# Performance work log

Hardware: AMD Instinct MI355X
Metric: run time of the kernel (lower is better)

Reference implementation:

```python
import jax, jax.numpy as jnp
import numpy as np

TEMP = 0.025
BN_EPS = 1e-5


def _attention(a, W_in, b_in, g, beta, rm, rv, W_out, b_out):
    # a: (b, n1, n2, P, Q); 1x1 conv over the Q 'channel' dim, gate, softmax over P.
    m = a.mean(axis=3)                                   # (b,n1,n2,Q)
    t = jnp.einsum('bnmq,kq->bnmk', m, W_in) + b_in      # (b,n1,n2,K)
    t = jax.nn.relu((t - rm) / jnp.sqrt(rv + BN_EPS) * g + beta)
    t = jnp.einsum('bnmk,qk->bnmq', t, W_out) + b_out    # (b,n1,n2,Q)
    s = jnp.mean(a * t[:, :, :, None, :], axis=-1)       # (b,n1,n2,P)
    return jax.nn.softmax(s / TEMP, axis=-1) + 1.0


def _cam_forward(zf, xf, conv1_w, conv1_b, bn1_g, bn1_b, bn1_rm, bn1_rv,
                 conv2_w, conv2_b, conv3_w, conv3_b, bn3_g, bn3_b, bn3_rm, bn3_rv,
                 conv4_w, conv4_b):
    out1, out2 = [], []
    L = zf.shape[0]
    for l in range(L):  # small fixed loop over feature levels
        f1, f2 = zf[l], xf[l]
        b, c, h1, w1 = f1.shape
        h2, w2 = f2.shape[2], f2.shape[3]
        P, Q = h1 * w1, h2 * w2
        f1s = jnp.stack([f1.reshape(b, c, P)] * 2, axis=1)   # (b,2,c,P)
        f2s = jnp.stack([f2.reshape(b, c, Q)] * 2, axis=1)   # (b,2,c,Q)
        f1n = f1s / jnp.maximum(jnp.linalg.norm(f1s, axis=2, keepdims=True), 1e-12)
        f2n = f2s / jnp.maximum(jnp.linalg.norm(f2s, axis=2, keepdims=True), 1e-12)
        a1 = jnp.einsum('bncp,bmcq->bnmpq', f1n, f2n)        # (b,2,2,P,Q)
        att1 = _attention(a1, conv1_w, conv1_b, bn1_g, bn1_b, bn1_rm, bn1_rv,
                          conv2_w, conv2_b)                  # (b,2,2,P)
        att2 = _attention(a1.swapaxes(3, 4), conv3_w, conv3_b, bn3_g, bn3_b,
                          bn3_rm, bn3_rv, conv4_w, conv4_b)  # (b,2,2,Q)
        # mean over the (n1,n2)=(2,2) pair grid without materializing (b,2,2,c,HW)
        o1 = jnp.einsum('bncp,bnmp->bcp', f1s, att1) / 4.0
        o2 = jnp.einsum('bmcq,bnmq->bcq', f2s, att2) / 4.0
        out1.append(o1.reshape(b, c, h1, w1))
        out2.append(o2.reshape(b, c, h2, w2))
    return (jnp.stack(out1), jnp.stack(out2))


def setup_inputs() -> dict:
    key = jax.random.key(0)
    ks = jax.random.split(key, 12)
    L, B, C = 3, 32, 256
    inp = {
        'zf': jax.random.normal(ks[0], (L, B, C, 7, 7), jnp.float32),
        'xf': jax.random.normal(ks[1], (L, B, C, 31, 31), jnp.float32),
        'conv1_w': jax.random.normal(ks[2], (31, 961), jnp.float32) * np.sqrt(2.0 / 31),
        'conv1_b': jax.random.normal(ks[3], (31,), jnp.float32) * 0.05,
        'bn1_g': jax.random.uniform(ks[4], (31,), jnp.float32, 0.5, 1.5),
        'bn1_b': jax.random.normal(ks[5], (31,), jnp.float32) * 0.05,
        'bn1_rm': jnp.zeros((31,), jnp.float32),
        'bn1_rv': jnp.ones((31,), jnp.float32),
        'conv2_w': jax.random.normal(ks[6], (961, 31), jnp.float32) * np.sqrt(2.0 / 961),
        'conv2_b': jax.random.normal(ks[7], (961,), jnp.float32) * 0.05,
        'conv3_w': jax.random.normal(ks[8], (7, 49), jnp.float32) * np.sqrt(2.0 / 7),
        'conv3_b': jax.random.normal(ks[9], (7,), jnp.float32) * 0.05,
        'bn3_g': jax.random.uniform(ks[10], (7,), jnp.float32, 0.5, 1.5),
        'bn3_b': jax.random.normal(ks[11], (7,), jnp.float32) * 0.05,
        'bn3_rm': jnp.zeros((7,), jnp.float32),
        'bn3_rv': jnp.ones((7,), jnp.float32),
        'conv4_w': jax.random.normal(jax.random.fold_in(key, 100), (49, 7), jnp.float32) * np.sqrt(2.0 / 49),
        'conv4_b': jax.random.normal(jax.random.fold_in(key, 101), (49,), jnp.float32) * 0.05,
    }
    return inp


def reference(zf, xf, conv1_w, conv1_b, bn1_g, bn1_b, bn1_rm, bn1_rv,
              conv2_w, conv2_b, conv3_w, conv3_b, bn3_g, bn3_b, bn3_rm, bn3_rv,
              conv4_w, conv4_b):
    return _cam_forward(zf, xf, conv1_w, conv1_b, bn1_g, bn1_b, bn1_rm, bn1_rv,
                        conv2_w, conv2_b, conv3_w, conv3_b, bn3_g, bn3_b,
                        bn3_rm, bn3_rv, conv4_w, conv4_b)
```

## Files before the change

kernel.cpp:

```cpp
#include <hip/hip_runtime.h>
#include <math.h>

#define NLB 96
#define CC  256
#define PP  49
#define QQ  961
#define QP  1024
#define TEMP_INV 40.0f
#define BN_EPS 1e-5f

#define N1 (NLB*CC*PP)
#define N2 (NLB*CC*QQ)

__global__ __launch_bounds__(256) void prep_z(
    const float* __restrict__ zf, float* __restrict__ inv1_ws,
    float* __restrict__ w_ws)
{
    const int lb = blockIdx.x;
    const int tid = threadIdx.x;
    __shared__ float f1L[CC * PP];
    __shared__ float inv1L[PP];
    const float* __restrict__ f1 = zf + (size_t)lb * CC * PP;
    for (int i = tid; i < CC * PP; i += 256) f1L[i] = f1[i];
    __syncthreads();
    if (tid < PP) {
        float ss = 0.f;
        for (int c = 0; c < CC; ++c) { const float x = f1L[c * PP + tid]; ss = fmaf(x, x, ss); }
        const float iv = 1.0f / fmaxf(sqrtf(ss), 1e-12f);
        inv1L[tid] = iv;
        inv1_ws[lb * 64 + tid] = iv;
    }
    __syncthreads();
    {
        float s = 0.f;
#pragma unroll
        for (int p = 0; p < PP; ++p) s = fmaf(inv1L[p], f1L[tid * PP + p], s);
        w_ws[lb * CC + tid] = s;
    }
}

__global__ __launch_bounds__(256) void xpass1(
    const float* __restrict__ xf, const float* __restrict__ w_ws,
    float* __restrict__ ssp, float* __restrict__ dcp)
{
    const int qg = blockIdx.x;
    const int ch = blockIdx.y;
    const int lb = blockIdx.z;
    const int tid = threadIdx.x;
    const int q  = qg * 256 + tid;
    const bool qv = (q < QQ);
    const int qc = qv ? q : QQ - 1;

    __shared__ float wL[128];
    if (tid < 128) wL[tid] = w_ws[lb * CC + ch * 128 + tid];
    __syncthreads();

    const float* __restrict__ base =
        xf + (size_t)lb * CC * QQ + (size_t)(ch * 128) * QQ + qc;

    float ss = 0.f, dc = 0.f;
    for (int c0 = 0; c0 < 128; c0 += 16) {
        float x[16];
#pragma unroll
        for (int j = 0; j < 16; ++j) x[j] = base[(size_t)(c0 + j) * QQ];
#pragma unroll
        for (int j = 0; j < 16; ++j) {
            ss = fmaf(x[j], x[j], ss);
            dc = fmaf(wL[c0 + j], x[j], dc);
        }
    }
    if (qv) {
        ssp[((size_t)ch * NLB + lb) * QP + q] = ss;
        dcp[((size_t)ch * NLB + lb) * QP + q] = dc;
    }
}

__global__ __launch_bounds__(1024) void finq_kernel(
    const float* __restrict__ ssp, const float* __restrict__ dcp,
    float* __restrict__ inv2_ws, float* __restrict__ mcol_ws)
{
    const int lb = blockIdx.x;
    const int q = threadIdx.x;
    if (q >= QQ) return;
    const float ss = ssp[((size_t)0 * NLB + lb) * QP + q] +
                     ssp[((size_t)1 * NLB + lb) * QP + q];
    const float dc = dcp[((size_t)0 * NLB + lb) * QP + q] +
                     dcp[((size_t)1 * NLB + lb) * QP + q];
    const float iv2 = 1.0f / fmaxf(sqrtf(ss), 1e-12f);
    inv2_ws[lb * QP + q] = iv2;
    mcol_ws[lb * QP + q] = dc * iv2 * (1.0f / PP);
}

__global__ __launch_bounds__(512) void vpass_kernel(
    const float* __restrict__ xf, const float* __restrict__ wq_ws,
    float* __restrict__ vout_ws)
{
    const int cb = blockIdx.x;
    const int lb = blockIdx.y;
    const int tid  = threadIdx.x;
    const int lane = tid & 63;
    const int wave = tid >> 6;

    __shared__ float wqL[QP];
    for (int i = tid; i < QP; i += 512)
        wqL[i] = (i < QQ) ? wq_ws[lb * QP + i] : 0.f;
    __syncthreads();

    const float* __restrict__ f2 = xf + (size_t)lb * CC * QQ;

#pragma unroll
    for (int r = 0; r < 8; ++r) {
        const int c = cb * 64 + wave * 8 + r;
        const float* __restrict__ row = f2 + (size_t)c * QQ;
        float x[16];
#pragma unroll
        for (int j = 0; j < 16; ++j) {
            const int qi = j * 64 + lane;
            x[j] = row[qi < QQ ? qi : QQ - 1];
        }
        float s = 0.f;
#pragma unroll
        for (int j = 0; j < 16; ++j) s = fmaf(x[j], wqL[j * 64 + lane], s);
        for (int off = 32; off > 0; off >>= 1) s += __shfl_xor(s, off, 64);
        if (lane == 0) vout_ws[lb * CC + c] = s;
    }
}

__global__ __launch_bounds__(512) void mid_kernel(
    const float* __restrict__ zf, const float* __restrict__ v_ws,
    const float* __restrict__ inv1_ws, const float* __restrict__ mcol_ws,
    const float* __restrict__ inv2_ws,
    const float* __restrict__ W1, const float* __restrict__ b1,
    const float* __restrict__ g1, const float* __restrict__ bb1,
    const float* __restrict__ rm1, const float* __restrict__ rv1,
    const float* __restrict__ W2, const float* __restrict__ b2,
    const float* __restrict__ W3, const float* __restrict__ b3,
    const float* __restrict__ g3, const float* __restrict__ bb3,
    const float* __restrict__ rm3, const float* __restrict__ rv3,
    const float* __restrict__ W4, const float* __restrict__ b4,
    float* __restrict__ wgt_ws, float* __restrict__ wb_ws)
{
    const int lb = blockIdx.x;
    const int tid = threadIdx.x;
    __shared__ float f1L[CC * PP];
    __shared__ float inv1L[64], vL[CC], mrowL[PP];
    __shared__ float mcolL[QQ];
    __shared__ float taL[31], tbL[7], t2bL[PP];

    const float* __restrict__ f1 = zf + (size_t)lb * CC * PP;
    for (int i = tid; i < CC * PP; i += 512) f1L[i] = f1[i];
    if (tid < 64) inv1L[tid] = inv1_ws[lb * 64 + tid];
    if (tid >= 64 && tid < 64 + CC) vL[tid - 64] = v_ws[lb * CC + tid - 64];
    for (int q = tid; q < QQ; q += 512) mcolL[q] = mcol_ws[lb * QP + q];
    __syncthreads();

    if (tid < PP) {
        float s = 0.f;
        for (int c = 0; c < CC; ++c) s = fmaf(f1L[c * PP + tid], vL[c], s);
        mrowL[tid] = s * inv1L[tid] * (1.0f / QQ);
    }
    if (tid < 31 * 16) {
        const int k = tid >> 4, sub = tid & 15;
        float s = 0.f;
        for (int q = sub; q < QQ; q += 16) s = fmaf(mcolL[q], W1[k * QQ + q], s);
        s += __shfl_xor(s, 1, 64); s += __shfl_xor(s, 2, 64);
        s += __shfl_xor(s, 4, 64); s += __shfl_xor(s, 8, 64);
        if (sub == 0) {
            float t = s + b1[k];
            t = (t - rm1[k]) * rsqrtf(rv1[k] + BN_EPS) * g1[k] + bb1[k];
            taL[k] = fmaxf(t, 0.f);
        }
    }
    __syncthreads();
    if (tid < 7 * 8) {
        const int k = tid >> 3, sub = tid & 7;
        float s = 0.f;
        for (int p = sub; p < PP; p += 8) s = fmaf(mrowL[p], W3[k * PP + p], s);
        s += __shfl_xor(s, 1, 64); s += __shfl_xor(s, 2, 64); s += __shfl_xor(s, 4, 64);
        if (sub == 0) {
            float t = s + b3[k];
            t = (t - rm3[k]) * rsqrtf(rv3[k] + BN_EPS) * g3[k] + bb3[k];
            tbL[k] = fmaxf(t, 0.f);
        }
    }
    __syncthreads();
    if (tid < PP) {
        float s = b4[tid];
#pragma unroll
        for (int k = 0; k < 7; ++k) s = fmaf(tbL[k], W4[tid * 7 + k], s);
        t2bL[tid] = s;
    }
    for (int q = tid; q < QQ; q += 512) {
        float s = b2[q];
#pragma unroll
        for (int k = 0; k < 31; ++k) s = fmaf(taL[k], W2[q * 31 + k], s);
        wgt_ws[lb * QP + q] = s * inv2_ws[lb * QP + q];
    }
    __syncthreads();
    if (tid < CC) {
        float s = 0.f;
#pragma unroll
        for (int p = 0; p < PP; ++p) s = fmaf(inv1L[p] * t2bL[p], f1L[tid * PP + p], s);
        wb_ws[lb * CC + tid] = s;
    }
}

__global__ __launch_bounds__(256) void xjoint(
    const float* __restrict__ xf, const float* __restrict__ wb_ws,
    const float* __restrict__ wgt_ws,
    float* __restrict__ s2p, float* __restrict__ vbp)
{
    const int qg = blockIdx.x;
    const int ch = blockIdx.y;
    const int lb = blockIdx.z;
    const int tid  = threadIdx.x;
    const int lane = tid & 63;
    const int wave = tid >> 6;
    const int q  = qg * 256 + tid;
    const bool qv = (q < QQ);
    const int qc = qv ? q : QQ - 1;

    __shared__ float wbL[128];
    __shared__ float wgtL[256];
    __shared__ __align__(16) float tile[16 * 264];

    if (tid < 128) wbL[tid] = wb_ws[lb * CC + ch * 128 + tid];
    wgtL[tid] = qv ? wgt_ws[lb * QP + q] : 0.f;

    const float* __restrict__ base =
        xf + (size_t)lb * CC * QQ + (size_t)(ch * 128) * QQ + qc;
    float* __restrict__ vbpo = vbp + ((size_t)(lb * 4 + qg)) * CC + ch * 128;

    float dwb = 0.f;
    for (int c0 = 0; c0 < 128; c0 += 16) {
        __syncthreads();
#pragma unroll
        for (int r = 0; r < 16; ++r)
            tile[r * 264 + tid] = base[(size_t)(c0 + r) * QQ];
        __syncthreads();
#pragma unroll
        for (int r = 0; r < 16; ++r)
            dwb = fmaf(wbL[c0 + r], tile[r * 264 + tid], dwb);
#pragma unroll
        for (int rr = 0; rr < 4; ++rr) {
            const int r = wave + rr * 4;
            float s = 0.f;
#pragma unroll
            for (int j = 0; j < 4; ++j)
                s = fmaf(tile[r * 264 + j * 64 + lane], wgtL[j * 64 + lane], s);
            for (int off = 32; off > 0; off >>= 1) s += __shfl_xor(s, off, 64);
            if (lane == 0) vbpo[c0 + r] = s;
        }
    }
    if (qv) s2p[((size_t)ch * NLB + lb) * QP + q] = dwb;
}

__global__ __launch_bounds__(512) void fin_kernel(
    const float* __restrict__ zf, const float* __restrict__ vbp,
    const float* __restrict__ inv1_ws, const float* __restrict__ s2p,
    const float* __restrict__ inv2_ws,
    float* __restrict__ att1_ws, float* __restrict__ att2_ws)
{
    const int lb = blockIdx.x;
    const int tid = threadIdx.x;
    const int lane = tid & 63;
    const int wv = tid >> 6;
    __shared__ float f1L[CC * PP];
    __shared__ float vbL[CC], inv1L[64], s1L[PP];
    __shared__ float s2L[QQ];
    __shared__ float redM[8], redS[8];

    const float* __restrict__ f1 = zf + (size_t)lb * CC * PP;
    for (int i = tid; i < CC * PP; i += 512) f1L[i] = f1[i];
    if (tid < CC) {
        float s = 0.f;
#pragma unroll
        for (int qg = 0; qg < 4; ++qg)
            s += vbp[((size_t)(lb * 4 + qg)) * CC + tid];
        vbL[tid] = s;
    }
    if (tid >= 256 && tid < 320) inv1L[tid - 256] = inv1_ws[lb * 64 + tid - 256];
    for (int q = tid; q < QQ; q += 512)
        s2L[q] = (s2p[((size_t)0 * NLB + lb) * QP + q] +
                  s2p[((size_t)1 * NLB + lb) * QP + q]) *
                 inv2_ws[lb * QP + q] * (1.0f / PP) * TEMP_INV;
    __syncthreads();

    if (tid < PP) {
        float s = 0.f;
        for (int c = 0; c < CC; ++c) s = fmaf(f1L[c * PP + tid], vbL[c], s);
        s1L[tid] = s * inv1L[tid] * (1.0f / QQ) * TEMP_INV;
    }
    __syncthreads();

    if (wv == 0) {
        const float v = (lane < PP) ? s1L[lane] : -3.4e38f;
        float m = v;
        for (int off = 32; off > 0; off >>= 1) m = fmaxf(m, __shfl_xor(m, off, 64));
        const float e = (lane < PP) ? expf(v - m) : 0.f;
        float sum = e;
        for (int off = 32; off > 0; off >>= 1) sum += __shfl_xor(sum, off, 64);
        if (lane < PP) att1_ws[lb * PP + lane] = e / sum + 1.0f;
    }

    float lm = -3.4e38f;
    for (int q = tid; q < QQ; q += 512) lm = fmaxf(lm, s2L[q]);
    for (int off = 32; off > 0; off >>= 1) lm = fmaxf(lm, __shfl_xor(lm, off, 64));
    if (lane == 0) redM[wv] = lm;
    __syncthreads();
    float gm = redM[0];
#pragma unroll
    for (int i = 1; i < 8; ++i) gm = fmaxf(gm, redM[i]);
    float ls = 0.f;
    for (int q = tid; q < QQ; q += 512) ls += expf(s2L[q] - gm);
    for (int off = 32; off > 0; off >>= 1) ls += __shfl_xor(ls, off, 64);
    if (lane == 0) redS[wv] = ls;
    __syncthreads();
    float tot = 0.f;
#pragma unroll
    for (int i = 0; i < 8; ++i) tot += redS[i];
    const float rinv = 1.0f / tot;
    for (int q = tid; q < QQ; q += 512)
        att2_ws[lb * QQ + q] = expf(s2L[q] - gm) * rinv + 1.0f;
}

template <int INNER>
__global__ __launch_bounds__(256) void scale_kernel(
    const float* __restrict__ in, const float* __restrict__ att,
    float* __restrict__ out, int n4)
{
    const int i = blockIdx.x * 256 + threadIdx.x;
    if (i >= n4) return;
    const float4 v = reinterpret_cast<const float4*>(in)[i];
    const float* vv = reinterpret_cast<const float*>(&v);
    float4 o;
    float* ov = reinterpret_cast<float*>(&o);
    const int g = i * 4;
#pragma unroll
    for (int j = 0; j < 4; ++j) {
        const int gg = g + j;
        const int lb = gg / (CC * INNER);
        const int x  = gg % INNER;
        ov[j] = vv[j] * att[lb * INNER + x];
    }
    reinterpret_cast<float4*>(out)[i] = o;
}

extern "C" void kernel_launch(void* const* d_in, const int* in_sizes, int n_in,
                              void* d_out, int out_size, void* d_ws, size_t ws_size,
                              hipStream_t stream)
{
    const float* zf  = (const float*)d_in[0];
    const float* xf  = (const float*)d_in[1];
    const float* W1  = (const float*)d_in[2];
    const float* b1  = (const float*)d_in[3];
    const float* g1  = (const float*)d_in[4];
    const float* bb1 = (const float*)d_in[5];
    const float* rm1 = (const float*)d_in[6];
    const float* rv1 = (const float*)d_in[7];
    const float* W2  = (const float*)d_in[8];
    const float* b2  = (const float*)d_in[9];
    const float* W3  = (const float*)d_in[10];
    const float* b3  = (const float*)d_in[11];
    const float* g3  = (const float*)d_in[12];
    const float* bb3 = (const float*)d_in[13];
    const float* rm3 = (const float*)d_in[14];
    const float* rv3 = (const float*)d_in[15];
    const float* W4  = (const float*)d_in[16];
    const float* b4  = (const float*)d_in[17];

    float* ws = (float*)d_ws;
    float* w    = ws;
    float* v    = w    + (size_t)NLB * CC;
    float* wb   = v    + (size_t)NLB * CC;
    float* inv1 = wb   + (size_t)NLB * CC;
    float* inv2 = inv1 + (size_t)NLB * 64;
    float* mcol = inv2 + (size_t)NLB * QP;
    float* wgt  = mcol + (size_t)NLB * QP;
    float* att1 = wgt  + (size_t)NLB * QP;
    float* att2 = att1 + (size_t)NLB * PP;
    float* ssp  = att2 + (size_t)NLB * QQ;
    float* dcp  = ssp  + (size_t)2 * NLB * QP;
    float* s2p  = dcp  + (size_t)2 * NLB * QP;
    float* vbp  = s2p  + (size_t)2 * NLB * QP;

    float* out1 = (float*)d_out;
    float* out2 = out1 + N1;

    prep_z<<<NLB, 256, 0, stream>>>(zf, inv1, w);

    dim3 gqs(4, 2, NLB);
    xpass1<<<gqs, 256, 0, stream>>>(xf, w, ssp, dcp);
    finq_kernel<<<NLB, 1024, 0, stream>>>(ssp, dcp, inv2, mcol);

    dim3 gv(4, NLB);
    vpass_kernel<<<gv, 512, 0, stream>>>(xf, inv2, v);

    mid_kernel<<<NLB, 512, 0, stream>>>(zf, v, inv1, mcol, inv2,
        W1, b1, g1, bb1, rm1, rv1, W2, b2,
        W3, b3, g3, bb3, rm3, rv3, W4, b4,
        wgt, wb);

    xjoint<<<gqs, 256, 0, stream>>>(xf, wb, wgt, s2p, vbp);

    fin_kernel<<<NLB, 512, 0, stream>>>(zf, vbp, inv1, s2p, inv2, att1, att2);

    const int n4_1 = N1 / 4;
    const int n4_2 = N2 / 4;
    scale_kernel<PP><<<(n4_1 + 255) / 256, 256, 0, stream>>>(zf, att1, out1, n4_1);
    scale_kernel<QQ><<<(n4_2 + 255) / 256, 256, 0, stream>>>(xf, att2, out2, n4_2);
}
```

Measured before the change: 133.8 us.

## Fuse x-norm pass, finalize and v-pass into one kernel per q-slice

Replaces xpass1, finq_kernel and vpass_kernel with a single xjoint1 kernel in which each block covers a 256-wide q slice across all 256 channels. The block computes the norms and mcol directly, then re-reads xf (likely from cache) to form partial v sums per q group, which mid_kernel adds up. This removes two launches and the partial-sum round trips, but cuts the grid to 384 blocks with a serial loop over 256 channels, which may lower parallelism. The vbp layout in xjoint and fin_kernel is also reindexed.

New measurement: 143.5 us. +7.3%, slower.

```diff
diff --git a/kernel.cpp b/kernel.cpp
--- a/kernel.cpp
+++ b/kernel.cpp
@@ -39,95 +39,72 @@
     }
 }
 
-__global__ __launch_bounds__(256) void xpass1(
+__global__ __launch_bounds__(256) void xjoint1(
     const float* __restrict__ xf, const float* __restrict__ w_ws,
-    float* __restrict__ ssp, float* __restrict__ dcp)
+    float* __restrict__ inv2_ws, float* __restrict__ mcol_ws,
+    float* __restrict__ vp)
 {
     const int qg = blockIdx.x;
-    const int ch = blockIdx.y;
-    const int lb = blockIdx.z;
-    const int tid = threadIdx.x;
-    const int q  = qg * 256 + tid;
-    const bool qv = (q < QQ);
-    const int qc = qv ? q : QQ - 1;
-
-    __shared__ float wL[128];
-    if (tid < 128) wL[tid] = w_ws[lb * CC + ch * 128 + tid];
-    __syncthreads();
-
-    const float* __restrict__ base =
-        xf + (size_t)lb * CC * QQ + (size_t)(ch * 128) * QQ + qc;
-
-    float ss = 0.f, dc = 0.f;
-    for (int c0 = 0; c0 < 128; c0 += 16) {
-        float x[16];
-#pragma unroll
-        for (int j = 0; j < 16; ++j) x[j] = base[(size_t)(c0 + j) * QQ];
-#pragma unroll
-        for (int j = 0; j < 16; ++j) {
-            ss = fmaf(x[j], x[j], ss);
-            dc = fmaf(wL[c0 + j], x[j], dc);
-        }
-    }
-    if (qv) {
-        ssp[((size_t)ch * NLB + lb) * QP + q] = ss;
-        dcp[((size_t)ch * NLB + lb) * QP + q] = dc;
-    }
-}
-
-__global__ __launch_bounds__(1024) void finq_kernel(
-    const float* __restrict__ ssp, const float* __restrict__ dcp,
-    float* __restrict__ inv2_ws, float* __restrict__ mcol_ws)
-{
-    const int lb = blockIdx.x;
-    const int q = threadIdx.x;
-    if (q >= QQ) return;
-    const float ss = ssp[((size_t)0 * NLB + lb) * QP + q] +
-                     ssp[((size_t)1 * NLB + lb) * QP + q];
-    const float dc = dcp[((size_t)0 * NLB + lb) * QP + q] +
-                     dcp[((size_t)1 * NLB + lb) * QP + q];
-    const float iv2 = 1.0f / fmaxf(sqrtf(ss), 1e-12f);
-    inv2_ws[lb * QP + q] = iv2;
-    mcol_ws[lb * QP + q] = dc * iv2 * (1.0f / PP);
-}
-
-__global__ __launch_bounds__(512) void vpass_kernel(
-    const float* __restrict__ xf, const float* __restrict__ wq_ws,
-    float* __restrict__ vout_ws)
-{
-    const int cb = blockIdx.x;
     const int lb = blockIdx.y;
     const int tid  = threadIdx.x;
     const int lane = tid & 63;
     const int wave = tid >> 6;
-
-    __shared__ float wqL[QP];
-    for (int i = tid; i < QP; i += 512)
-        wqL[i] = (i < QQ) ? wq_ws[lb * QP + i] : 0.f;
-    __syncthreads();
-
-    const float* __restrict__ f2 = xf + (size_t)lb * CC * QQ;
-
-#pragma unroll
-    for (int r = 0; r < 8; ++r) {
-        const int c = cb * 64 + wave * 8 + r;
-        const float* __restrict__ row = f2 + (size_t)c * QQ;
-        float x[16];
-#pragma unroll
-        for (int j = 0; j < 16; ++j) {
-            const int qi = j * 64 + lane;
-            x[j] = row[qi < QQ ? qi : QQ - 1];
-        }
-        float s = 0.f;
-#pragma unroll
-        for (int j = 0; j < 16; ++j) s = fmaf(x[j], wqL[j * 64 + lane], s);
-        for (int off = 32; off > 0; off >>= 1) s += __shfl_xor(s, off, 64);
-        if (lane == 0) vout_ws[lb * CC + c] = s;
+    const int q  = qg * 256 + tid;
+    const bool qv = (q < QQ);
+    const int qc = qv ? q : QQ - 1;
+
+    __shared__ float wL[CC];
+    __shared__ float wqL[256];
+    __shared__ __align__(16) float tile[16 * 264];
+
+    wL[tid] = w_ws[lb * CC + tid];
+
+    const float* __restrict__ base = xf + (size_t)lb * CC * QQ + qc;
+
+    float ss = 0.f, dc = 0.f;
+    for (int c0 = 0; c0 < CC; c0 += 16) {
+        __syncthreads();
+#pragma unroll
+        for (int r = 0; r < 16; ++r)
+            tile[r * 264 + tid] = base[(size_t)(c0 + r) * QQ];
+        __syncthreads();
+#pragma unroll
+        for (int r = 0; r < 16; ++r) {
+            const float x = tile[r * 264 + tid];
+            ss = fmaf(x, x, ss);
+            dc = fmaf(wL[c0 + r], x, dc);
+        }
+    }
+    const float iv2 = 1.0f / fmaxf(sqrtf(ss), 1e-12f);
+    if (qv) {
+        inv2_ws[lb * QP + q] = iv2;
+        mcol_ws[lb * QP + q] = dc * iv2 * (1.0f / PP);
+    }
+    __syncthreads();
+    wqL[tid] = qv ? iv2 : 0.f;
+
+    float* __restrict__ vpo = vp + ((size_t)(lb * 4 + qg)) * CC;
+    for (int c0 = 0; c0 < CC; c0 += 16) {
+        __syncthreads();
+#pragma unroll
+        for (int r = 0; r < 16; ++r)
+            tile[r * 264 + tid] = base[(size_t)(c0 + r) * QQ];
+        __syncthreads();
+#pragma unroll
+        for (int rr = 0; rr < 4; ++rr) {
+            const int r = wave + rr * 4;
+            float s = 0.f;
+#pragma unroll
+            for (int j = 0; j < 4; ++j)
+                s = fmaf(tile[r * 264 + j * 64 + lane], wqL[j * 64 + lane], s);
+            for (int off = 32; off > 0; off >>= 1) s += __shfl_xor(s, off, 64);
+            if (lane == 0) vpo[c0 + r] = s;
+        }
     }
 }
 
 __global__ __launch_bounds__(512) void mid_kernel(
-    const float* __restrict__ zf, const float* __restrict__ v_ws,
+    const float* __restrict__ zf, const float* __restrict__ vp,
     const float* __restrict__ inv1_ws, const float* __restrict__ mcol_ws,
     const float* __restrict__ inv2_ws,
     const float* __restrict__ W1, const float* __restrict__ b1,
@@ -150,7 +127,12 @@
     const float* __restrict__ f1 = zf + (size_t)lb * CC * PP;
     for (int i = tid; i < CC * PP; i += 512) f1L[i] = f1[i];
     if (tid < 64) inv1L[tid] = inv1_ws[lb * 64 + tid];
-    if (tid >= 64 && tid < 64 + CC) vL[tid - 64] = v_ws[lb * CC + tid - 64];
+    if (tid < CC) {
+        float s = 0.f;
+#pragma unroll
+        for (int qg = 0; qg < 4; ++qg) s += vp[((size_t)(lb * 4 + qg)) * CC + tid];
+        vL[tid] = s;
+    }
     for (int q = tid; q < QQ; q += 512) mcolL[q] = mcol_ws[lb * QP + q];
     __syncthreads();
 
@@ -229,7 +211,7 @@
 
     const float* __restrict__ base =
         xf + (size_t)lb * CC * QQ + (size_t)(ch * 128) * QQ + qc;
-    float* __restrict__ vbpo = vbp + ((size_t)(lb * 4 + qg)) * CC + ch * 128;
+    float* __restrict__ vbpo = vbp + ((size_t)(lb * 8 + ch * 4 + qg)) * 128;
 
     float dwb = 0.f;
     for (int c0 = 0; c0 < 128; c0 += 16) {
@@ -273,10 +255,12 @@
     const float* __restrict__ f1 = zf + (size_t)lb * CC * PP;
     for (int i = tid; i < CC * PP; i += 512) f1L[i] = f1[i];
     if (tid < CC) {
+        const int ch = tid >> 7;
+        const int co = tid & 127;
         float s = 0.f;
 #pragma unroll
         for (int qg = 0; qg < 4; ++qg)
-            s += vbp[((size_t)(lb * 4 + qg)) * CC + tid];
+            s += vbp[((size_t)(lb * 8 + ch * 4 + qg)) * 128 + co];
         vbL[tid] = s;
     }
     if (tid >= 256 && tid < 320) inv1L[tid - 256] = inv1_ws[lb * 64 + tid - 256];
@@ -371,36 +355,31 @@
 
     float* ws = (float*)d_ws;
     float* w    = ws;
-    float* v    = w    + (size_t)NLB * CC;
-    float* wb   = v    + (size_t)NLB * CC;
+    float* wb   = w    + (size_t)NLB * CC;
     float* inv1 = wb   + (size_t)NLB * CC;
     float* inv2 = inv1 + (size_t)NLB * 64;
     float* mcol = inv2 + (size_t)NLB * QP;
     float* wgt  = mcol + (size_t)NLB * QP;
     float* att1 = wgt  + (size_t)NLB * QP;
     float* att2 = att1 + (size_t)NLB * PP;
-    float* ssp  = att2 + (size_t)NLB * QQ;
-    float* dcp  = ssp  + (size_t)2 * NLB * QP;
-    float* s2p  = dcp  + (size_t)2 * NLB * QP;
-    float* vbp  = s2p  + (size_t)2 * NLB * QP;
+    float* s2p  = att2 + (size_t)NLB * QQ;
+    float* vp   = s2p  + (size_t)2 * NLB * QP;
+    float* vbp  = vp   + (size_t)NLB * 4 * CC;
 
     float* out1 = (float*)d_out;
     float* out2 = out1 + N1;
 
     prep_z<<<NLB, 256, 0, stream>>>(zf, inv1, w);
 
-    dim3 gqs(4, 2, NLB);
-    xpass1<<<gqs, 256, 0, stream>>>(xf, w, ssp, dcp);
-    finq_kernel<<<NLB, 1024, 0, stream>>>(ssp, dcp, inv2, mcol);
-
-    dim3 gv(4, NLB);
-    vpass_kernel<<<gv, 512, 0, stream>>>(xf, inv2, v);
-
-    mid_kernel<<<NLB, 512, 0, stream>>>(zf, v, inv1, mcol, inv2,
+    dim3 g1q(4, NLB);
+    xjoint1<<<g1q, 256, 0, stream>>>(xf, w, inv2, mcol, vp);
+
+    mid_kernel<<<NLB, 512, 0, stream>>>(zf, vp, inv1, mcol, inv2,
         W1, b1, g1, bb1, rm1, rv1, W2, b2,
         W3, b3, g3, bb3, rm3, rv3, W4, b4,
         wgt, wb);
 
+    dim3 gqs(4, 2, NLB);
     xjoint<<<gqs, 256, 0, stream>>>(xf, wb, wgt, s2p, vbp);
 
     fin_kernel<<<NLB, 512, 0, stream>>>(zf, vbp, inv1, s2p, inv2, att1, att2);
```
